# Kernel tuning notes

Hardware: AMD Instinct MI355X
Metric: run time of the kernel (lower is better)

## Reference

```python
import jax, jax.numpy as jnp
import numpy as np

ALPHA = 100.0
ETA_0 = 0.3
SIGMA_0 = 16.0  # max(map shape)/2


def setup_inputs() -> dict:
    key = jax.random.key(0)
    k1, k2 = jax.random.split(key)
    Z = jax.random.normal(k1, (512, 256), dtype=jnp.float32)
    SOM = jax.random.uniform(k2, (32, 32, 256), dtype=jnp.float32)  # 'random_uniform' init
    return {"Z": Z, "SOM": SOM, "step": 0}


def reference(Z, SOM, step):
    """NeuralMap.call(training=True, iter=1): one SOM update + KL loss.

    Z:   [B, E] batch of embeddings
    SOM: [H, W, E] map weights
    Returns (kl_loss [B], delta [B, H, W, E]) matching the returned dict values.
    """
    H, W, E = SOM.shape
    B = Z.shape[0]
    n = jnp.asarray(step, dtype=jnp.float32)
    eta = ETA_0 * jnp.exp(-n / ALPHA)          # learning rate eta(n)
    sigma = SIGMA_0 * jnp.exp(-n / ALPHA)      # neighborhood radius sigma(n)

    # --- best_match_neuron: broadcast diff + L2 norm over embed dim + argmin ---
    diff = Z[:, None, None, :] - SOM[None]                      # [B, H, W, E]
    dist = jnp.sqrt(jnp.sum(diff * diff, axis=-1))              # [B, H, W]
    u_flat = jnp.argmin(dist.reshape(B, -1), axis=-1)           # [B]

    # lattice index grid [H, W, 2]
    grid = jnp.stack(
        jnp.meshgrid(jnp.arange(H), jnp.arange(W), indexing="ij"), axis=-1
    )
    U = grid.reshape(-1, 2)[u_flat]                              # [B, 2] BMU indices

    # --- neighborhood function H(u, j)(n) over the whole lattice ---
    idx_diff = (U[:, None, None, :] - grid[None]).astype(jnp.float32)  # [B, H, W, 2]
    h = jnp.exp(-jnp.sum(idx_diff * idx_diff, axis=-1) / (2.0 * sigma * sigma))

    # --- delta = eta(n) * H * (Z - w_j), update_memory('average') ---
    delta = eta * h[..., None] * diff                            # [B, H, W, E]
    SOM_new = SOM + jnp.mean(delta, axis=0)

    # --- get_kl_loss on the updated map ---
    Wf = SOM_new.reshape(-1, E)                                  # [H*W, E]
    d = jnp.sqrt(jnp.sum((Z[:, None, :] - Wf[None]) ** 2, axis=-1))  # [B, H*W]
    raw_q = 1.0 / (1.0 + d)
    q = raw_q / jnp.sum(raw_q, axis=-1, keepdims=True)           # [B, L]
    raw_p = (q * q) / jnp.sum(q, axis=0, keepdims=True)
    p = raw_p / jnp.sum(raw_p, axis=1, keepdims=True)
    kl_loss = jnp.sum(p * jnp.log(p / q), axis=-1)               # [B]

    return kl_loss, delta
```

## Files before the change

### kernel.cpp

```cpp
#include <hip/hip_runtime.h>
#include <math.h>

#define B 512
#define E 256
#define L 1024

typedef float f32x4 __attribute__((ext_vector_type(4)));
typedef unsigned long long u64;

#define O_Q     0u
#define O_SOMN  524288u
#define O_PART  786432u
#define O_PRS   802816u
#define O_H     811008u
#define O_BMUP  1335296u

__global__ __launch_bounds__(256) void dist_bmu_kernel(const float* __restrict__ Zg,
                                                       const float* __restrict__ Wg,
                                                       u64* __restrict__ bmupart) {
    __shared__ float Zs[32][67];
    __shared__ float Ws[64][67];
    __shared__ u64 red[32][16];
    const int tid = threadIdx.x;
    const int tb = blockIdx.x >> 4;
    const int tn = blockIdx.x & 15;
    const int b0 = tb * 32, n0 = tn * 64;
    const int ty = tid >> 4, tx = tid & 15;

    float acc[2][4];
#pragma unroll
    for (int i = 0; i < 2; ++i)
#pragma unroll
        for (int j = 0; j < 4; ++j) acc[i][j] = 0.f;

    for (int kc = 0; kc < E; kc += 64) {
        const int c4 = tx * 4;
#pragma unroll
        for (int s = 0; s < 2; ++s) {
            const int r = ty + 16 * s;
            float4 zv = *(const float4*)(Zg + (size_t)(b0 + r) * E + kc + c4);
            Zs[r][c4 + 0] = zv.x; Zs[r][c4 + 1] = zv.y;
            Zs[r][c4 + 2] = zv.z; Zs[r][c4 + 3] = zv.w;
        }
#pragma unroll
        for (int s = 0; s < 4; ++s) {
            const int r = ty + 16 * s;
            float4 wv = *(const float4*)(Wg + (size_t)(n0 + r) * E + kc + c4);
            Ws[r][c4 + 0] = wv.x; Ws[r][c4 + 1] = wv.y;
            Ws[r][c4 + 2] = wv.z; Ws[r][c4 + 3] = wv.w;
        }
        __syncthreads();
#pragma unroll 4
        for (int k = 0; k < 64; ++k) {
            float zr[2], wr[4];
#pragma unroll
            for (int i = 0; i < 2; ++i) zr[i] = Zs[ty * 2 + i][k];
#pragma unroll
            for (int j = 0; j < 4; ++j) wr[j] = Ws[tx * 4 + j][k];
#pragma unroll
            for (int i = 0; i < 2; ++i)
#pragma unroll
                for (int j = 0; j < 4; ++j) {
                    float d = zr[i] - wr[j];
                    acc[i][j] = fmaf(d, d, acc[i][j]);
                }
        }
        __syncthreads();
    }
#pragma unroll
    for (int i = 0; i < 2; ++i) {
        float best = acc[i][0];
        int bj = 0;
#pragma unroll
        for (int j = 1; j < 4; ++j)
            if (acc[i][j] < best) { best = acc[i][j]; bj = j; }
        red[ty * 2 + i][tx] = ((u64)__float_as_uint(best) << 32) |
                              (unsigned)(n0 + tx * 4 + bj);
    }
    __syncthreads();
    if (tid < 32) {
        u64 m = red[tid][0];
#pragma unroll
        for (int t = 1; t < 16; ++t) {
            const u64 v = red[tid][t];
            if (v < m) m = v;
        }
        bmupart[(size_t)tn * B + b0 + tid] = m;
    }
}

__global__ __launch_bounds__(256) void h_kernel(const u64* __restrict__ bmupart,
                                                const int* __restrict__ step,
                                                float* __restrict__ h) {
    const int b = blockIdx.x;
    u64 m = bmupart[b];
#pragma unroll
    for (int tn = 1; tn < 16; ++tn) {
        const u64 v = bmupart[(size_t)tn * B + b];
        if (v < m) m = v;
    }
    const int u = (int)(m & 0xffffffffULL);
    const int ur = u >> 5, uc = u & 31;
    const float n = (float)step[0];
    const float decay = expf(-n * 0.01f);
    const float eta = 0.3f * decay;
    const float sigma = 16.0f * decay;
    const float inv2s2 = 1.0f / (2.0f * sigma * sigma);
#pragma unroll
    for (int s = 0; s < 4; ++s) {
        const int t = threadIdx.x + s * 256;
        const int i = t >> 5, j = t & 31;
        const float dr = (float)(ur - i), dc = (float)(uc - j);
        h[(size_t)b * L + t] = eta * expf(-(dr * dr + dc * dc) * inv2s2);
    }
}

__global__ __launch_bounds__(256) void delta_update_kernel(const float* __restrict__ Zg,
                                                           const float* __restrict__ Wg,
                                                           const float* __restrict__ h,
                                                           float* __restrict__ somn,
                                                           float* __restrict__ delta) {
    if (blockIdx.x < 1024) {
        const int hw = blockIdx.x;
        const int e = threadIdx.x;
        float acc = 0.f, hsum = 0.f;
#pragma unroll 8
        for (int b = 0; b < B; ++b) {
            const float hv = h[(size_t)b * L + hw];
            acc = fmaf(hv, Zg[(size_t)b * E + e], acc);
            hsum += hv;
        }
        const float w = Wg[(size_t)hw * E + e];
        somn[(size_t)hw * E + e] = w + (1.0f / (float)B) * (acc - hsum * w);
        return;
    }
    const int bid = blockIdx.x - 1024;
    const int b = bid >> 8;
    const int hw = ((bid & 255) << 2) + (threadIdx.x >> 6);
    const int lane = threadIdx.x & 63;
    const float hs = h[(size_t)b * L + hw];
    const float4 z = *(const float4*)(Zg + (size_t)b * E + lane * 4);
    const float4 w = *(const float4*)(Wg + (size_t)hw * E + lane * 4);
    f32x4 o;
    o.x = hs * (z.x - w.x);
    o.y = hs * (z.y - w.y);
    o.z = hs * (z.z - w.z);
    o.w = hs * (z.w - w.w);
    __builtin_nontemporal_store(o, (f32x4*)(delta + ((size_t)b * L + hw) * E + lane * 4));
}

__global__ __launch_bounds__(256) void distq_kernel(const float* __restrict__ Zg,
                                                    const float* __restrict__ Wg,
                                                    float* __restrict__ out,
                                                    float* __restrict__ part_rs) {
    __shared__ float Zs[32][67];
    __shared__ float Ws[64][67];
    __shared__ float red[32][16];
    const int tid = threadIdx.x;
    const int tb = blockIdx.x >> 4;
    const int tn = blockIdx.x & 15;
    const int b0 = tb * 32, n0 = tn * 64;
    const int ty = tid >> 4, tx = tid & 15;

    float acc[2][4];
#pragma unroll
    for (int i = 0; i < 2; ++i)
#pragma unroll
        for (int j = 0; j < 4; ++j) acc[i][j] = 0.f;

    for (int kc = 0; kc < E; kc += 64) {
        const int c4 = tx * 4;
#pragma unroll
        for (int s = 0; s < 2; ++s) {
            const int r = ty + 16 * s;
            float4 zv = *(const float4*)(Zg + (size_t)(b0 + r) * E + kc + c4);
            Zs[r][c4 + 0] = zv.x; Zs[r][c4 + 1] = zv.y;
            Zs[r][c4 + 2] = zv.z; Zs[r][c4 + 3] = zv.w;
        }
#pragma unroll
        for (int s = 0; s < 4; ++s) {
            const int r = ty + 16 * s;
            float4 wv = *(const float4*)(Wg + (size_t)(n0 + r) * E + kc + c4);
            Ws[r][c4 + 0] = wv.x; Ws[r][c4 + 1] = wv.y;
            Ws[r][c4 + 2] = wv.z; Ws[r][c4 + 3] = wv.w;
        }
        __syncthreads();
#pragma unroll 4
        for (int k = 0; k < 64; ++k) {
            float zr[2], wr[4];
#pragma unroll
            for (int i = 0; i < 2; ++i) zr[i] = Zs[ty * 2 + i][k];
#pragma unroll
            for (int j = 0; j < 4; ++j) wr[j] = Ws[tx * 4 + j][k];
#pragma unroll
            for (int i = 0; i < 2; ++i)
#pragma unroll
                for (int j = 0; j < 4; ++j) {
                    float d = zr[i] - wr[j];
                    acc[i][j] = fmaf(d, d, acc[i][j]);
                }
        }
        __syncthreads();
    }
#pragma unroll
    for (int i = 0; i < 2; ++i) {
        const int b = b0 + ty * 2 + i;
        float4 v;
        v.x = 1.f / (1.f + sqrtf(acc[i][0]));
        v.y = 1.f / (1.f + sqrtf(acc[i][1]));
        v.z = 1.f / (1.f + sqrtf(acc[i][2]));
        v.w = 1.f / (1.f + sqrtf(acc[i][3]));
        *(float4*)(out + (size_t)b * L + n0 + tx * 4) = v;
        red[ty * 2 + i][tx] = v.x + v.y + v.z + v.w;
    }
    __syncthreads();
    if (tid < 32) {
        float s = red[tid][0];
#pragma unroll
        for (int t = 1; t < 16; ++t) s += red[tid][t];
        part_rs[(size_t)tn * B + b0 + tid] = s;
    }
}

__global__ __launch_bounds__(256) void colsum_part_kernel(const float* __restrict__ q,
                                                          const float* __restrict__ prs,
                                                          float* __restrict__ part) {
    __shared__ float sirs[32];
    const int j = (blockIdx.x & 3) * 256 + threadIdx.x;
    const int c = blockIdx.x >> 2;
    const int b0 = c * 32;
    if (threadIdx.x < 32) {
        float s = 0.f;
#pragma unroll
        for (int tn = 0; tn < 16; ++tn) s += prs[(size_t)tn * B + b0 + threadIdx.x];
        sirs[threadIdx.x] = 1.0f / s;
    }
    __syncthreads();
    float acc = 0.f;
#pragma unroll 8
    for (int bo = 0; bo < 32; ++bo)
        acc = fmaf(q[(size_t)(b0 + bo) * L + j], sirs[bo], acc);
    part[(size_t)c * L + j] = acc;
}

__global__ __launch_bounds__(256) void kl_kernel(const float* __restrict__ q,
                                                 const float* __restrict__ prs,
                                                 const float* __restrict__ part,
                                                 float* __restrict__ kl) {
    const int b = blockIdx.x;
    const int tid = threadIdx.x;
    float rs = 0.f;
#pragma unroll
    for (int tn = 0; tn < 16; ++tn) rs += prs[(size_t)tn * B + b];
    const float irsb = 1.0f / rs;
    float S = 0.f, T = 0.f;
#pragma unroll
    for (int s = 0; s < 4; ++s) {
        const int j = tid + s * 256;
        float csj = 0.f;
#pragma unroll
        for (int c = 0; c < 16; ++c) csj += part[(size_t)c * L + j];
        const float qq = q[(size_t)b * L + j] * irsb;
        const float ic = 1.0f / csj;
        const float rp = qq * qq * ic;
        S += rp;
        T = fmaf(rp, logf(qq * ic), T);
    }
    __shared__ float sS[256], sT[256];
    sS[tid] = S; sT[tid] = T;
    __syncthreads();
    for (int st = 128; st > 0; st >>= 1) {
        if (tid < st) { sS[tid] += sS[tid + st]; sT[tid] += sT[tid + st]; }
        __syncthreads();
    }
    if (tid == 0) kl[b] = sT[0] / sS[0] - logf(sS[0]);
}

extern "C" void kernel_launch(void* const* d_in, const int* in_sizes, int n_in,
                              void* d_out, int out_size, void* d_ws, size_t ws_size,
                              hipStream_t stream) {
    const float* Zg = (const float*)d_in[0];
    const float* Wg = (const float*)d_in[1];
    const int* step = (const int*)d_in[2];
    float* out = (float*)d_out;
    float* ws = (float*)d_ws;

    float* q    = ws + O_Q;
    float* somn = ws + O_SOMN;
    float* part = ws + O_PART;
    float* prs  = ws + O_PRS;
    float* h    = ws + O_H;
    u64*   bmup = (u64*)(ws + O_BMUP);

    float* kl    = out;
    float* delta = out + B;

    hipLaunchKernelGGL(dist_bmu_kernel, dim3(256), dim3(256), 0, stream, Zg, Wg, bmup);
    hipLaunchKernelGGL(h_kernel, dim3(B), dim3(256), 0, stream, bmup, step, h);
    hipLaunchKernelGGL(delta_update_kernel, dim3(1024 + B * 256), dim3(256), 0, stream,
                       Zg, Wg, h, somn, delta);
    hipLaunchKernelGGL(distq_kernel, dim3(256), dim3(256), 0, stream, Zg, somn, q, prs);
    hipLaunchKernelGGL(colsum_part_kernel, dim3(64), dim3(256), 0, stream, q, prs, part);
    hipLaunchKernelGGL(kl_kernel, dim3(B), dim3(256), 0, stream, q, prs, part, kl);
}
```

Measured before the change: 132.9 us.

## Split delta writes across later kernels to overlap with KL stages

The large delta store (B*L*E floats) is split by batch rows: rows 0-383 stay in the first update kernel, and rows 384-511 are appended as extra blocks to the distance/q, column-sum and KL kernels. Each of those small, latency-bound stages now shares a launch with bandwidth-bound delta blocks, so the GPU is not underutilised during them. The risk is that the heavy delta blocks slow down the critical-path compute blocks in the same launch. The combined distq kernel also uses more shared memory per block, including for the delta-only blocks.

```diff
diff --git a/kernel.cpp b/kernel.cpp
--- a/kernel.cpp
+++ b/kernel.cpp
@@ -14,6 +14,25 @@
 #define O_PRS   802816u
 #define O_H     811008u
 #define O_BMUP  1335296u
+
+__device__ __forceinline__ void delta_body(int bid, int bbase, int tid,
+                                           const float* __restrict__ Zg,
+                                           const float* __restrict__ Wg,
+                                           const float* __restrict__ h,
+                                           float* __restrict__ delta) {
+    const int b = bbase + (bid >> 8);
+    const int hw = ((bid & 255) << 2) + (tid >> 6);
+    const int lane = tid & 63;
+    const float hs = h[(size_t)b * L + hw];
+    const float4 z = *(const float4*)(Zg + (size_t)b * E + lane * 4);
+    const float4 w = *(const float4*)(Wg + (size_t)hw * E + lane * 4);
+    f32x4 o;
+    o.x = hs * (z.x - w.x);
+    o.y = hs * (z.y - w.y);
+    o.z = hs * (z.z - w.z);
+    o.w = hs * (z.w - w.w);
+    __builtin_nontemporal_store(o, (f32x4*)(delta + ((size_t)b * L + hw) * E + lane * 4));
+}
 
 __global__ __launch_bounds__(256) void dist_bmu_kernel(const float* __restrict__ Zg,
                                                        const float* __restrict__ Wg,
@@ -115,11 +134,11 @@
     }
 }
 
-__global__ __launch_bounds__(256) void delta_update_kernel(const float* __restrict__ Zg,
-                                                           const float* __restrict__ Wg,
-                                                           const float* __restrict__ h,
-                                                           float* __restrict__ somn,
-                                                           float* __restrict__ delta) {
+__global__ __launch_bounds__(256) void mega1_kernel(const float* __restrict__ Zg,
+                                                    const float* __restrict__ Wg,
+                                                    const float* __restrict__ h,
+                                                    float* __restrict__ somn,
+                                                    float* __restrict__ delta) {
     if (blockIdx.x < 1024) {
         const int hw = blockIdx.x;
         const int e = threadIdx.x;
@@ -134,146 +153,158 @@
         somn[(size_t)hw * E + e] = w + (1.0f / (float)B) * (acc - hsum * w);
         return;
     }
-    const int bid = blockIdx.x - 1024;
-    const int b = bid >> 8;
-    const int hw = ((bid & 255) << 2) + (threadIdx.x >> 6);
-    const int lane = threadIdx.x & 63;
-    const float hs = h[(size_t)b * L + hw];
-    const float4 z = *(const float4*)(Zg + (size_t)b * E + lane * 4);
-    const float4 w = *(const float4*)(Wg + (size_t)hw * E + lane * 4);
-    f32x4 o;
-    o.x = hs * (z.x - w.x);
-    o.y = hs * (z.y - w.y);
-    o.z = hs * (z.z - w.z);
-    o.w = hs * (z.w - w.w);
-    __builtin_nontemporal_store(o, (f32x4*)(delta + ((size_t)b * L + hw) * E + lane * 4));
-}
-
-__global__ __launch_bounds__(256) void distq_kernel(const float* __restrict__ Zg,
+    delta_body(blockIdx.x - 1024, 0, threadIdx.x, Zg, Wg, h, delta);
+}
+
+__global__ __launch_bounds__(256) void mega2_kernel(const float* __restrict__ Zg,
                                                     const float* __restrict__ Wg,
-                                                    float* __restrict__ out,
-                                                    float* __restrict__ part_rs) {
-    __shared__ float Zs[32][67];
-    __shared__ float Ws[64][67];
-    __shared__ float red[32][16];
-    const int tid = threadIdx.x;
-    const int tb = blockIdx.x >> 4;
-    const int tn = blockIdx.x & 15;
-    const int b0 = tb * 32, n0 = tn * 64;
-    const int ty = tid >> 4, tx = tid & 15;
-
-    float acc[2][4];
-#pragma unroll
-    for (int i = 0; i < 2; ++i)
-#pragma unroll
-        for (int j = 0; j < 4; ++j) acc[i][j] = 0.f;
-
-    for (int kc = 0; kc < E; kc += 64) {
-        const int c4 = tx * 4;
-#pragma unroll
-        for (int s = 0; s < 2; ++s) {
-            const int r = ty + 16 * s;
-            float4 zv = *(const float4*)(Zg + (size_t)(b0 + r) * E + kc + c4);
-            Zs[r][c4 + 0] = zv.x; Zs[r][c4 + 1] = zv.y;
-            Zs[r][c4 + 2] = zv.z; Zs[r][c4 + 3] = zv.w;
-        }
+                                                    const float* __restrict__ somn,
+                                                    const float* __restrict__ h,
+                                                    float* __restrict__ q,
+                                                    float* __restrict__ prs,
+                                                    float* __restrict__ delta) {
+    __shared__ float smem[32 * 67 + 64 * 67 + 32 * 16];
+    if (blockIdx.x < 256) {
+        float(*Zs)[67] = (float(*)[67])smem;
+        float(*Ws)[67] = (float(*)[67])(smem + 32 * 67);
+        float(*red)[16] = (float(*)[16])(smem + 32 * 67 + 64 * 67);
+        const int tid = threadIdx.x;
+        const int tb = blockIdx.x >> 4;
+        const int tn = blockIdx.x & 15;
+        const int b0 = tb * 32, n0 = tn * 64;
+        const int ty = tid >> 4, tx = tid & 15;
+
+        float acc[2][4];
+#pragma unroll
+        for (int i = 0; i < 2; ++i)
+#pragma unroll
+            for (int j = 0; j < 4; ++j) acc[i][j] = 0.f;
+
+        for (int kc = 0; kc < E; kc += 64) {
+            const int c4 = tx * 4;
+#pragma unroll
+            for (int s = 0; s < 2; ++s) {
+                const int r = ty + 16 * s;
+                float4 zv = *(const float4*)(Zg + (size_t)(b0 + r) * E + kc + c4);
+                Zs[r][c4 + 0] = zv.x; Zs[r][c4 + 1] = zv.y;
+                Zs[r][c4 + 2] = zv.z; Zs[r][c4 + 3] = zv.w;
+            }
+#pragma unroll
+            for (int s = 0; s < 4; ++s) {
+                const int r = ty + 16 * s;
+                float4 wv = *(const float4*)(somn + (size_t)(n0 + r) * E + kc + c4);
+                Ws[r][c4 + 0] = wv.x; Ws[r][c4 + 1] = wv.y;
+                Ws[r][c4 + 2] = wv.z; Ws[r][c4 + 3] = wv.w;
+            }
+            __syncthreads();
+#pragma unroll 4
+            for (int k = 0; k < 64; ++k) {
+                float zr[2], wr[4];
+#pragma unroll
+                for (int i = 0; i < 2; ++i) zr[i] = Zs[ty * 2 + i][k];
+#pragma unroll
+                for (int j = 0; j < 4; ++j) wr[j] = Ws[tx * 4 + j][k];
+#pragma unroll
+                for (int i = 0; i < 2; ++i)
+#pragma unroll
+                    for (int j = 0; j < 4; ++j) {
+                        float d = zr[i] - wr[j];
+                        acc[i][j] = fmaf(d, d, acc[i][j]);
+                    }
+            }
+            __syncthreads();
+        }
+#pragma unroll
+        for (int i = 0; i < 2; ++i) {
+            const int b = b0 + ty * 2 + i;
+            float4 v;
+            v.x = 1.f / (1.f + sqrtf(acc[i][0]));
+            v.y = 1.f / (1.f + sqrtf(acc[i][1]));
+            v.z = 1.f / (1.f + sqrtf(acc[i][2]));
+            v.w = 1.f / (1.f + sqrtf(acc[i][3]));
+            *(float4*)(q + (size_t)b * L + n0 + tx * 4) = v;
+            red[ty * 2 + i][tx] = v.x + v.y + v.z + v.w;
+        }
+        __syncthreads();
+        if (tid < 32) {
+            float s = red[tid][0];
+#pragma unroll
+            for (int t = 1; t < 16; ++t) s += red[tid][t];
+            prs[(size_t)tn * B + b0 + tid] = s;
+        }
+        return;
+    }
+    delta_body(blockIdx.x - 256, 384, threadIdx.x, Zg, Wg, h, delta);
+}
+
+__global__ __launch_bounds__(256) void mega3_kernel(const float* __restrict__ Zg,
+                                                    const float* __restrict__ Wg,
+                                                    const float* __restrict__ h,
+                                                    const float* __restrict__ q,
+                                                    const float* __restrict__ prs,
+                                                    float* __restrict__ part,
+                                                    float* __restrict__ delta) {
+    if (blockIdx.x < 64) {
+        __shared__ float sirs[32];
+        const int j = (blockIdx.x & 3) * 256 + threadIdx.x;
+        const int c = blockIdx.x >> 2;
+        const int b0 = c * 32;
+        if (threadIdx.x < 32) {
+            float s = 0.f;
+#pragma unroll
+            for (int tn = 0; tn < 16; ++tn) s += prs[(size_t)tn * B + b0 + threadIdx.x];
+            sirs[threadIdx.x] = 1.0f / s;
+        }
+        __syncthreads();
+        float acc = 0.f;
+#pragma unroll 8
+        for (int bo = 0; bo < 32; ++bo)
+            acc = fmaf(q[(size_t)(b0 + bo) * L + j], sirs[bo], acc);
+        part[(size_t)c * L + j] = acc;
+        return;
+    }
+    delta_body(blockIdx.x - 64, 448, threadIdx.x, Zg, Wg, h, delta);
+}
+
+__global__ __launch_bounds__(256) void mega4_kernel(const float* __restrict__ Zg,
+                                                    const float* __restrict__ Wg,
+                                                    const float* __restrict__ h,
+                                                    const float* __restrict__ q,
+                                                    const float* __restrict__ prs,
+                                                    const float* __restrict__ part,
+                                                    float* __restrict__ kl,
+                                                    float* __restrict__ delta) {
+    if (blockIdx.x < 512) {
+        __shared__ float sS[256], sT[256];
+        const int b = blockIdx.x;
+        const int tid = threadIdx.x;
+        float rs = 0.f;
+#pragma unroll
+        for (int tn = 0; tn < 16; ++tn) rs += prs[(size_t)tn * B + b];
+        const float irsb = 1.0f / rs;
+        float S = 0.f, T = 0.f;
 #pragma unroll
         for (int s = 0; s < 4; ++s) {
-            const int r = ty + 16 * s;
-            float4 wv = *(const float4*)(Wg + (size_t)(n0 + r) * E + kc + c4);
-            Ws[r][c4 + 0] = wv.x; Ws[r][c4 + 1] = wv.y;
-            Ws[r][c4 + 2] = wv.z; Ws[r][c4 + 3] = wv.w;
-        }
-        __syncthreads();
-#pragma unroll 4
-        for (int k = 0; k < 64; ++k) {
-            float zr[2], wr[4];
-#pragma unroll
-            for (int i = 0; i < 2; ++i) zr[i] = Zs[ty * 2 + i][k];
-#pragma unroll
-            for (int j = 0; j < 4; ++j) wr[j] = Ws[tx * 4 + j][k];
-#pragma unroll
-            for (int i = 0; i < 2; ++i)
-#pragma unroll
-                for (int j = 0; j < 4; ++j) {
-                    float d = zr[i] - wr[j];
-                    acc[i][j] = fmaf(d, d, acc[i][j]);
-                }
-        }
-        __syncthreads();
-    }
-#pragma unroll
-    for (int i = 0; i < 2; ++i) {
-        const int b = b0 + ty * 2 + i;
-        float4 v;
-        v.x = 1.f / (1.f + sqrtf(acc[i][0]));
-        v.y = 1.f / (1.f + sqrtf(acc[i][1]));
-        v.z = 1.f / (1.f + sqrtf(acc[i][2]));
-        v.w = 1.f / (1.f + sqrtf(acc[i][3]));
-        *(float4*)(out + (size_t)b * L + n0 + tx * 4) = v;
-        red[ty * 2 + i][tx] = v.x + v.y + v.z + v.w;
-    }
-    __syncthreads();
-    if (tid < 32) {
-        float s = red[tid][0];
-#pragma unroll
-        for (int t = 1; t < 16; ++t) s += red[tid][t];
-        part_rs[(size_t)tn * B + b0 + tid] = s;
-    }
-}
-
-__global__ __launch_bounds__(256) void colsum_part_kernel(const float* __restrict__ q,
-                                                          const float* __restrict__ prs,
-                                                          float* __restrict__ part) {
-    __shared__ float sirs[32];
-    const int j = (blockIdx.x & 3) * 256 + threadIdx.x;
-    const int c = blockIdx.x >> 2;
-    const int b0 = c * 32;
-    if (threadIdx.x < 32) {
-        float s = 0.f;
-#pragma unroll
-        for (int tn = 0; tn < 16; ++tn) s += prs[(size_t)tn * B + b0 + threadIdx.x];
-        sirs[threadIdx.x] = 1.0f / s;
-    }
-    __syncthreads();
-    float acc = 0.f;
-#pragma unroll 8
-    for (int bo = 0; bo < 32; ++bo)
-        acc = fmaf(q[(size_t)(b0 + bo) * L + j], sirs[bo], acc);
-    part[(size_t)c * L + j] = acc;
-}
-
-__global__ __launch_bounds__(256) void kl_kernel(const float* __restrict__ q,
-                                                 const float* __restrict__ prs,
-                                                 const float* __restrict__ part,
-                                                 float* __restrict__ kl) {
-    const int b = blockIdx.x;
-    const int tid = threadIdx.x;
-    float rs = 0.f;
-#pragma unroll
-    for (int tn = 0; tn < 16; ++tn) rs += prs[(size_t)tn * B + b];
-    const float irsb = 1.0f / rs;
-    float S = 0.f, T = 0.f;
-#pragma unroll
-    for (int s = 0; s < 4; ++s) {
-        const int j = tid + s * 256;
-        float csj = 0.f;
-#pragma unroll
-        for (int c = 0; c < 16; ++c) csj += part[(size_t)c * L + j];
-        const float qq = q[(size_t)b * L + j] * irsb;
-        const float ic = 1.0f / csj;
-        const float rp = qq * qq * ic;
-        S += rp;
-        T = fmaf(rp, logf(qq * ic), T);
-    }
-    __shared__ float sS[256], sT[256];
-    sS[tid] = S; sT[tid] = T;
-    __syncthreads();
-    for (int st = 128; st > 0; st >>= 1) {
-        if (tid < st) { sS[tid] += sS[tid + st]; sT[tid] += sT[tid + st]; }
-        __syncthreads();
-    }
-    if (tid == 0) kl[b] = sT[0] / sS[0] - logf(sS[0]);
+            const int j = tid + s * 256;
+            float csj = 0.f;
+#pragma unroll
+            for (int c = 0; c < 16; ++c) csj += part[(size_t)c * L + j];
+            const float qq = q[(size_t)b * L + j] * irsb;
+            const float ic = 1.0f / csj;
+            const float rp = qq * qq * ic;
+            S += rp;
+            T = fmaf(rp, logf(qq * ic), T);
+        }
+        sS[tid] = S; sT[tid] = T;
+        __syncthreads();
+        for (int st = 128; st > 0; st >>= 1) {
+            if (tid < st) { sS[tid] += sS[tid + st]; sT[tid] += sT[tid + st]; }
+            __syncthreads();
+        }
+        if (tid == 0) kl[b] = sT[0] / sS[0] - logf(sS[0]);
+        return;
+    }
+    delta_body(blockIdx.x - 512, 480, threadIdx.x, Zg, Wg, h, delta);
 }
 
 extern "C" void kernel_launch(void* const* d_in, const int* in_sizes, int n_in,
@@ -297,9 +328,12 @@
 
     hipLaunchKernelGGL(dist_bmu_kernel, dim3(256), dim3(256), 0, stream, Zg, Wg, bmup);
     hipLaunchKernelGGL(h_kernel, dim3(B), dim3(256), 0, stream, bmup, step, h);
-    hipLaunchKernelGGL(delta_update_kernel, dim3(1024 + B * 256), dim3(256), 0, stream,
+    hipLaunchKernelGGL(mega1_kernel, dim3(1024 + 384 * 256), dim3(256), 0, stream,
                        Zg, Wg, h, somn, delta);
-    hipLaunchKernelGGL(distq_kernel, dim3(256), dim3(256), 0, stream, Zg, somn, q, prs);
-    hipLaunchKernelGGL(colsum_part_kernel, dim3(64), dim3(256), 0, stream, q, prs, part);
-    hipLaunchKernelGGL(kl_kernel, dim3(B), dim3(256), 0, stream, q, prs, part, kl);
-}
+    hipLaunchKernelGGL(mega2_kernel, dim3(256 + 64 * 256), dim3(256), 0, stream,
+                       Zg, Wg, somn, h, q, prs, delta);
+    hipLaunchKernelGGL(mega3_kernel, dim3(64 + 32 * 256), dim3(256), 0, stream,
+                       Zg, Wg, h, q, prs, part, delta);
+    hipLaunchKernelGGL(mega4_kernel, dim3(512 + 32 * 256), dim3(256), 0, stream,
+                       Zg, Wg, h, q, prs, part, kl, delta);
+}
```

Measured after the change: 118.7 us. 10.7% less time.
